# Kernel tuning notes

Measured on AMD Instinct MI355X. Metric: run time of the kernel, lower is better.

The kernel has to match this reference:

```python
import jax, jax.numpy as jnp
import numpy as np

DIM = 1024
NUM_HEADS = 16
HEAD_DIM = DIM // NUM_HEADS
SCALE = HEAD_DIM ** -0.5


def setup_inputs() -> dict:
    key = jax.random.key(0)
    ks = jax.random.split(key, 7)
    b, n = 2, 2048
    x = jax.random.normal(ks[0], (b, n, DIM), dtype=jnp.float32)
    s = DIM ** -0.5
    Wq = jax.random.normal(ks[1], (DIM, DIM), dtype=jnp.float32) * s
    bq = jax.random.normal(ks[2], (DIM,), dtype=jnp.float32) * 0.01
    Wk = jax.random.normal(ks[3], (DIM, DIM), dtype=jnp.float32) * s
    bk = jax.random.normal(ks[4], (DIM,), dtype=jnp.float32) * 0.01
    Wv = jax.random.normal(ks[5], (DIM, DIM), dtype=jnp.float32) * s
    bv = jax.random.normal(ks[6], (DIM,), dtype=jnp.float32) * 0.01
    return {"x": x, "Wq": Wq, "bq": bq, "Wk": Wk, "bk": bk, "Wv": Wv, "bv": bv}


def reference(x, Wq, bq, Wk, bk, Wv, bv):
    b, n, _ = x.shape
    # Linear projections (torch Linear: x @ W.T + b; here W stored as [in, out])
    q = x @ Wq + bq
    k = x @ Wk + bk
    v = x @ Wv + bv
    # split heads: [b, n, h*d] -> [b, h, n, d]
    split = lambda t: t.reshape(b, n, NUM_HEADS, HEAD_DIM).transpose(0, 2, 1, 3)
    q, k, v = split(q), split(k), split(v)
    sim = jnp.einsum('bhid,bhjd->bhij', q, k) * SCALE
    attn = jax.nn.softmax(sim, axis=-1)
    out = jnp.einsum('bhij,bhjd->bhid', attn, v)
    return out.transpose(0, 2, 1, 3).reshape(b, n, DIM)
```

## Files before the change

### kernel.cpp

```cpp
#include <hip/hip_runtime.h>
#include <cstdint>
#include <cstddef>

#define NB    2
#define SEQ   2048
#define DIMC  1024
#define NH    16
#define HDIM  64
#define MROWS (NB*SEQ)
#define NFEAT (3*DIMC)
#define KVBLK 64

typedef _Float16 half8 __attribute__((ext_vector_type(8)));
typedef _Float16 half4 __attribute__((ext_vector_type(4)));
typedef _Float16 half2v __attribute__((ext_vector_type(2)));
typedef __fp16   fp16x2 __attribute__((ext_vector_type(2)));
typedef float    f32x4 __attribute__((ext_vector_type(4)));

typedef const __attribute__((address_space(1))) void* gas_ptr;
typedef __attribute__((address_space(3))) void*       las_ptr;

__device__ __forceinline__ void gload_lds16(const void* g, void* l) {
    __builtin_amdgcn_global_load_lds((gas_ptr)g, (las_ptr)l, 16, 0, 0);
}

__device__ __forceinline__ int swz4(int r) { return (r ^ (r >> 2)) & 3; }

__device__ __forceinline__ float fast_exp2(float x) {
    float r;
    asm("v_exp_f32 %0, %1" : "=v"(r) : "v"(x));
    return r;
}

__device__ __forceinline__ half2v pk_f16(float a, float b) {
    fp16x2 r = __builtin_amdgcn_cvt_pkrtz(a, b);
    return __builtin_bit_cast(half2v, r);
}

__global__ __launch_bounds__(256) void k_prep(const float* __restrict__ x,
                                              const float* __restrict__ Wq,
                                              const float* __restrict__ Wk,
                                              const float* __restrict__ Wv,
                                              _Float16* __restrict__ x16,
                                              _Float16* __restrict__ wt) {
    __shared__ float tile[64][65];
    const int tid = threadIdx.x;
    if (blockIdx.x < 4096) {
        int i = (blockIdx.x * 256 + tid) * 4;
        float4 v = *reinterpret_cast<const float4*>(x + i);
        half4 h = { (_Float16)v.x, (_Float16)v.y, (_Float16)v.z, (_Float16)v.w };
        *reinterpret_cast<half4*>(x16 + i) = h;
        return;
    }
    const int bid  = blockIdx.x - 4096;
    const int midx = bid >> 8;
    const int t2   = bid & 255;
    const int i0   = (t2 >> 4) * 64;
    const int o0   = (t2 & 15) * 64;
    const float* W = (midx == 0) ? Wq : (midx == 1 ? Wk : Wv);
    #pragma unroll
    for (int p = 0; p < 4; ++p) {
        int id = p * 256 + tid;
        int r = id >> 4, c4 = (id & 15) * 4;
        float4 v = *reinterpret_cast<const float4*>(W + (size_t)(i0 + r) * DIMC + o0 + c4);
        tile[r][c4 + 0] = v.x; tile[r][c4 + 1] = v.y;
        tile[r][c4 + 2] = v.z; tile[r][c4 + 3] = v.w;
    }
    __syncthreads();
    #pragma unroll
    for (int p = 0; p < 4; ++p) {
        int id = p * 256 + tid;
        int oc = id >> 4, i4 = (id & 15) * 4;
        half4 h = { (_Float16)tile[i4 + 0][oc], (_Float16)tile[i4 + 1][oc],
                    (_Float16)tile[i4 + 2][oc], (_Float16)tile[i4 + 3][oc] };
        *reinterpret_cast<half4*>(wt + (size_t)(midx * DIMC + o0 + oc) * DIMC + i0 + i4) = h;
    }
}

__global__ __launch_bounds__(256) void k_qkv_gemm(
    const _Float16* __restrict__ x16, const _Float16* __restrict__ wt,
    const float* __restrict__ bq, const float* __restrict__ bk, const float* __restrict__ bv,
    _Float16* __restrict__ q16, _Float16* __restrict__ k16, _Float16* __restrict__ vt16)
{
    __shared__ __align__(16) char sraw[49152];
    const int tid = threadIdx.x;
    const int lane = tid & 63;
    const int w = tid >> 6, wm = w >> 1, wn = w & 1;
    const int lr = lane & 15, lg = lane >> 4;
    const int swzb = (blockIdx.x & 7) * 96 + (blockIdx.x >> 3);
    const int bn = swzb % (NFEAT / 128);
    const int bm = swzb / (NFEAT / 128);
    const int m0 = bm * 128, n0 = bn * 128;

    const f32x4 zero4 = {0.f, 0.f, 0.f, 0.f};
    f32x4 acc[4][4];
    #pragma unroll
    for (int i = 0; i < 4; ++i)
        #pragma unroll
        for (int j = 0; j < 4; ++j) acc[i][j] = zero4;

    auto stage = [&](int buf, int kt) {
        const int k0 = kt * 32;
        char* Adst = sraw + buf * 8192;
        char* Bdst = sraw + 24576 + buf * 8192;
        #pragma unroll
        for (int t = 0; t < 2; ++t) {
            int slot = t * 256 + tid;
            int row = slot >> 2, ch = slot & 3;
            int chg = ch ^ swz4(row);
            gload_lds16(x16 + (size_t)(m0 + row) * DIMC + k0 + chg * 8, Adst + slot * 16);
            gload_lds16(wt  + (size_t)(n0 + row) * DIMC + k0 + chg * 8, Bdst + slot * 16);
        }
    };

    stage(0, 0);
    stage(1, 1);
    for (int kt = 0; kt < DIMC / 32; ++kt) {
        if (kt < DIMC / 32 - 1) asm volatile("s_waitcnt vmcnt(4)" ::: "memory");
        else                    asm volatile("s_waitcnt vmcnt(0)" ::: "memory");
        __builtin_amdgcn_s_barrier();
        if (kt + 2 < DIMC / 32) stage((kt + 2) % 3, kt + 2);
        const char* Ab = sraw + (kt % 3) * 8192;
        const char* Bb = sraw + 24576 + (kt % 3) * 8192;
        half8 af[4], bf[4];
        #pragma unroll
        for (int mb = 0; mb < 4; ++mb) {
            int row = wm * 64 + mb * 16 + lr;
            af[mb] = *(const half8*)(Ab + row * 64 + ((lg ^ swz4(row)) << 4));
        }
        #pragma unroll
        for (int nb = 0; nb < 4; ++nb) {
            int col = wn * 64 + nb * 16 + lr;
            bf[nb] = *(const half8*)(Bb + col * 64 + ((lg ^ swz4(col)) << 4));
        }
        #pragma unroll
        for (int mb = 0; mb < 4; ++mb)
            #pragma unroll
            for (int nb = 0; nb < 4; ++nb)
                acc[mb][nb] = __builtin_amdgcn_mfma_f32_16x16x32_f16(af[mb], bf[nb], acc[mb][nb], 0, 0, 0);
    }

    const int sec = n0 >> 10;
    const float* bias = (sec == 0) ? bq : (sec == 1 ? bk : bv);
    const float scl = (sec == 0) ? 0.125f * 1.44269504088896f : 1.0f;
    float bfv[4];
    #pragma unroll
    for (int nb = 0; nb < 4; ++nb)
        bfv[nb] = bias[(n0 & 1023) + wn * 64 + nb * 16 + lr];

    if (sec < 2) {
        _Float16* dst = (sec == 0) ? q16 : k16;
        #pragma unroll
        for (int mb = 0; mb < 4; ++mb)
            #pragma unroll
            for (int i2 = 0; i2 < 4; ++i2) {
                int rg = m0 + wm * 64 + mb * 16 + lg * 4 + i2;
                int bb = rg >> 11, nn = rg & (SEQ - 1);
                #pragma unroll
                for (int nb = 0; nb < 4; ++nb) {
                    int f1 = (n0 & 1023) + wn * 64 + nb * 16 + lr;
                    int hh = f1 >> 6, dd = f1 & 63;
                    dst[((size_t)(bb * NH + hh) * SEQ + nn) * HDIM + dd] =
                        (_Float16)((acc[mb][nb][i2] + bfv[nb]) * scl);
                }
            }
    } else {
        __syncthreads();
        char* lt = sraw;
        #pragma unroll
        for (int mb = 0; mb < 4; ++mb)
            #pragma unroll
            for (int nb = 0; nb < 4; ++nb) {
                int c  = wn * 64 + nb * 16 + lr;
                int r0 = wm * 64 + mb * 16 + lg * 4;
                half4 hv = { (_Float16)(acc[mb][nb][0] + bfv[nb]),
                             (_Float16)(acc[mb][nb][1] + bfv[nb]),
                             (_Float16)(acc[mb][nb][2] + bfv[nb]),
                             (_Float16)(acc[mb][nb][3] + bfv[nb]) };
                *(half4*)(lt + c * 272 + r0 * 2) = hv;
            }
        __syncthreads();
        #pragma unroll
        for (int p = 0; p < 8; ++p) {
            int id = p * 256 + tid;
            int c = id >> 4, r8 = (id & 15) * 8;
            half8 hv = *(const half8*)(lt + c * 272 + r8 * 2);
            int f1 = (n0 & 1023) + c;
            int hh = f1 >> 6, dd = f1 & 63;
            int rg = m0 + r8;
            int bb = rg >> 11, nn = rg & (SEQ - 1);
            *(half8*)(vt16 + ((size_t)(bb * NH + hh) * HDIM + dd) * SEQ + nn) = hv;
        }
    }
}

__global__ __launch_bounds__(512, 4) void k_attn(
    const _Float16* __restrict__ q16, const _Float16* __restrict__ k16,
    const _Float16* __restrict__ vt16, float* __restrict__ out)
{
    __shared__ __align__(16) char lds[81920];
    const int tid = threadIdx.x, lane = tid & 63, w = tid >> 6;
    const int lr = lane & 15, lg = lane >> 4;
    const int sub = w >> 2;
    const int qg  = w & 3;
    const int swz = (blockIdx.x & 7) * 64 + (blockIdx.x >> 3);
    const int bh = swz >> 4;
    const int qt = swz & 15;
    const int qrow0 = qt * 128 + qg * 32;
    const _Float16* qh = q16 + (size_t)bh * SEQ * HDIM;
    const _Float16* kh = k16 + (size_t)bh * SEQ * HDIM;
    const _Float16* vh = vt16 + (size_t)bh * HDIM * SEQ;
    char* pl = lds + 65536 + w * 2048;
    const int rb = lr >> 3;

    const int srow = tid >> 3;
    const int scg  = (tid & 7) ^ (srow & 7);

    auto stageKV = [&](int buf, int t) {
        const int jA = t * KVBLK, jB = (16 + t) * KVBLK;
        gload_lds16(kh + (size_t)(jA + srow) * HDIM + scg * 8,
                    lds + buf * 8192 + tid * 16);
        gload_lds16(kh + (size_t)(jB + srow) * HDIM + scg * 8,
                    lds + 16384 + buf * 8192 + tid * 16);
        gload_lds16(vh + (size_t)srow * SEQ + jA + scg * 8,
                    lds + 32768 + buf * 8192 + tid * 16);
        gload_lds16(vh + (size_t)srow * SEQ + jB + scg * 8,
                    lds + 49152 + buf * 8192 + tid * 16);
    };

    half8 aq[2][2];
    #pragma unroll
    for (int g = 0; g < 2; ++g)
        #pragma unroll
        for (int kc = 0; kc < 2; ++kc)
            aq[g][kc] = *(const half8*)(qh + (size_t)(qrow0 + g * 16 + lr) * HDIM + kc * 32 + lg * 8);

    const f32x4 zero4 = {0.f, 0.f, 0.f, 0.f};
    f32x4 l4[2] = { zero4, zero4 };
    f32x4 oacc[2][4];
    #pragma unroll
    for (int g = 0; g < 2; ++g)
        #pragma unroll
        for (int i = 0; i < 4; ++i) oacc[g][i] = zero4;

    stageKV(0, 0);
    for (int t = 0; t < 16; ++t) {
        __syncthreads();
        if (t + 1 < 16) stageKV((t + 1) & 1, t + 1);
        const char* Kb = lds + sub * 16384 + (t & 1) * 8192;
        const char* Vb = lds + 32768 + sub * 16384 + (t & 1) * 8192;

        f32x4 s0[4], s1[4];
        __builtin_amdgcn_s_setprio(1);
        #pragma unroll
        for (int jb = 0; jb < 4; ++jb) {
            int row = jb * 16 + lr;
            half8 k0 = *(const half8*)(Kb + row * 128 + (((0 + lg) ^ (row & 7)) << 4));
            half8 k1 = *(const half8*)(Kb + row * 128 + (((4 + lg) ^ (row & 7)) << 4));
            f32x4 a0 = __builtin_amdgcn_mfma_f32_16x16x32_f16(k0, aq[0][0], zero4, 0, 0, 0);
            f32x4 a1 = __builtin_amdgcn_mfma_f32_16x16x32_f16(k0, aq[1][0], zero4, 0, 0, 0);
            a0 = __builtin_amdgcn_mfma_f32_16x16x32_f16(k1, aq[0][1], a0, 0, 0, 0);
            a1 = __builtin_amdgcn_mfma_f32_16x16x32_f16(k1, aq[1][1], a1, 0, 0, 0);
            s0[jb] = a0; s1[jb] = a1;
        }
        __builtin_amdgcn_s_setprio(0);

        #pragma unroll
        for (int jb = 0; jb < 4; ++jb) {
            #pragma unroll
            for (int i = 0; i < 4; ++i) s0[jb][i] = fast_exp2(s0[jb][i]);
            l4[0] += s0[jb];
            half2v w0 = pk_f16(s0[jb][0], s0[jb][1]);
            half2v w1 = pk_f16(s0[jb][2], s0[jb][3]);
            half4 pk = { w0.x, w0.y, w1.x, w1.y };
            *(half4*)(pl + lr * 128 + (((jb * 2 + (lg >> 1)) ^ (lr & 7)) << 4)
                      + (((lg & 1) ^ rb) << 3)) = pk;
        }
        half4 pk1[4];
        #pragma unroll
        for (int jb = 0; jb < 4; ++jb) {
            #pragma unroll
            for (int i = 0; i < 4; ++i) s1[jb][i] = fast_exp2(s1[jb][i]);
            l4[1] += s1[jb];
            half2v w0 = pk_f16(s1[jb][0], s1[jb][1]);
            half2v w1 = pk_f16(s1[jb][2], s1[jb][3]);
            pk1[jb] = half4{ w0.x, w0.y, w1.x, w1.y };
        }
        asm volatile("s_waitcnt lgkmcnt(0)" ::: "memory");
        const char* prow = pl + lr * 128;
        half8 ap[2][2];
        {
            half4 l0 = *(const half4*)(prow + (((0 + lg) ^ (lr & 7)) << 4) + (rb << 3));
            half4 h0 = *(const half4*)(prow + (((0 + lg) ^ (lr & 7)) << 4) + ((1 ^ rb) << 3));
            half4 l1 = *(const half4*)(prow + (((4 + lg) ^ (lr & 7)) << 4) + (rb << 3));
            half4 h1 = *(const half4*)(prow + (((4 + lg) ^ (lr & 7)) << 4) + ((1 ^ rb) << 3));
            ap[0][0] = half8{ l0.x, l0.y, l0.z, l0.w, h0.x, h0.y, h0.z, h0.w };
            ap[0][1] = half8{ l1.x, l1.y, l1.z, l1.w, h1.x, h1.y, h1.z, h1.w };
        }
        #pragma unroll
        for (int jb = 0; jb < 4; ++jb)
            *(half4*)(pl + lr * 128 + (((jb * 2 + (lg >> 1)) ^ (lr & 7)) << 4)
                      + (((lg & 1) ^ rb) << 3)) = pk1[jb];
        asm volatile("s_waitcnt lgkmcnt(0)" ::: "memory");
        {
            half4 l0 = *(const half4*)(prow + (((0 + lg) ^ (lr & 7)) << 4) + (rb << 3));
            half4 h0 = *(const half4*)(prow + (((0 + lg) ^ (lr & 7)) << 4) + ((1 ^ rb) << 3));
            half4 l1 = *(const half4*)(prow + (((4 + lg) ^ (lr & 7)) << 4) + (rb << 3));
            half4 h1 = *(const half4*)(prow + (((4 + lg) ^ (lr & 7)) << 4) + ((1 ^ rb) << 3));
            ap[1][0] = half8{ l0.x, l0.y, l0.z, l0.w, h0.x, h0.y, h0.z, h0.w };
            ap[1][1] = half8{ l1.x, l1.y, l1.z, l1.w, h1.x, h1.y, h1.z, h1.w };
        }
        __builtin_amdgcn_s_setprio(1);
        #pragma unroll
        for (int db = 0; db < 4; ++db) {
            int row = db * 16 + lr;
            half8 vf0 = *(const half8*)(Vb + row * 128 + (((0 + lg) ^ (row & 7)) << 4));
            half8 vf1 = *(const half8*)(Vb + row * 128 + (((4 + lg) ^ (row & 7)) << 4));
            oacc[0][db] = __builtin_amdgcn_mfma_f32_16x16x32_f16(ap[0][0], vf0, oacc[0][db], 0, 0, 0);
            oacc[1][db] = __builtin_amdgcn_mfma_f32_16x16x32_f16(ap[1][0], vf0, oacc[1][db], 0, 0, 0);
            oacc[0][db] = __builtin_amdgcn_mfma_f32_16x16x32_f16(ap[0][1], vf1, oacc[0][db], 0, 0, 0);
            oacc[1][db] = __builtin_amdgcn_mfma_f32_16x16x32_f16(ap[1][1], vf1, oacc[1][db], 0, 0, 0);
        }
        __builtin_amdgcn_s_setprio(0);
    }

    __syncthreads();
    char* xch = lds;
    if (sub == 1) {
        char* sl = xch + (qg * 2) * 5120;
        #pragma unroll
        for (int g = 0; g < 2; ++g) {
            #pragma unroll
            for (int db = 0; db < 4; ++db)
                *(f32x4*)(sl + g * 5120 + db * 1024 + lane * 16) = oacc[g][db];
            *(f32x4*)(sl + g * 5120 + 4096 + lane * 16) = l4[g];
        }
    }
    __syncthreads();
    if (sub == 0) {
        char* sl = xch + (qg * 2) * 5120;
        #pragma unroll
        for (int g = 0; g < 2; ++g) {
            #pragma unroll
            for (int db = 0; db < 4; ++db)
                oacc[g][db] += *(const f32x4*)(sl + g * 5120 + db * 1024 + lane * 16);
            l4[g] += *(const f32x4*)(sl + g * 5120 + 4096 + lane * 16);
        }
        const int bb = bh >> 4, hh = bh & 15;
        #pragma unroll
        for (int g = 0; g < 2; ++g) {
            float l_i = (l4[g][0] + l4[g][1]) + (l4[g][2] + l4[g][3]);
            l_i += __shfl_xor(l_i, 16);
            l_i += __shfl_xor(l_i, 32);
            float rlq[4];
            #pragma unroll
            for (int i = 0; i < 4; ++i)
                rlq[i] = 1.0f / __shfl(l_i, lg * 4 + i);
            #pragma unroll
            for (int db = 0; db < 4; ++db)
                #pragma unroll
                for (int i = 0; i < 4; ++i) {
                    int nn = qrow0 + g * 16 + lg * 4 + i;
                    out[((size_t)bb * SEQ + nn) * DIMC + hh * HDIM + db * 16 + lr] =
                        oacc[g][db][i] * rlq[i];
                }
        }
    }
}

extern "C" void kernel_launch(void* const* d_in, const int* in_sizes, int n_in,
                              void* d_out, int out_size, void* d_ws, size_t ws_size,
                              hipStream_t stream)
{
    const float* x  = (const float*)d_in[0];
    const float* Wq = (const float*)d_in[1];
    const float* bq = (const float*)d_in[2];
    const float* Wk = (const float*)d_in[3];
    const float* bk = (const float*)d_in[4];
    const float* Wv = (const float*)d_in[5];
    const float* bv = (const float*)d_in[6];
    float* out = (float*)d_out;

    char* ws = (char*)d_ws;
    _Float16* x16  = (_Float16*)ws;
    _Float16* wt   = (_Float16*)(ws + ((size_t)8  << 20));
    _Float16* q16  = (_Float16*)(ws + ((size_t)14 << 20));
    _Float16* k16  = (_Float16*)(ws + ((size_t)22 << 20));
    _Float16* vt16 = (_Float16*)(ws + ((size_t)30 << 20));

    k_prep<<<4096 + 768, 256, 0, stream>>>(x, Wq, Wk, Wv, x16, wt);
    k_qkv_gemm<<<(MROWS / 128) * (NFEAT / 128), 256, 0, stream>>>(x16, wt, bq, bk, bv,
                                                                  q16, k16, vt16);
    k_attn<<<32 * (SEQ / 128), 512, 0, stream>>>(q16, k16, vt16, out);
}
```

Before: 91.26 us.

## Enlarge QKV GEMM tiles to 256x256 with 8 waves and K=64 double buffering

Restructures the QKV projection GEMM so each 512-thread block computes a 256x256 output tile, staging K in chunks of 64 with double-buffered LDS and an 8-way XOR swizzle. Global loads for the next stage are interleaved with the MFMA sub-steps, and s_setprio raises wave priority around the MFMA bursts. The aim is more data reuse per LDS load and fewer blocks and barriers per unit of work. In exchange it uses 128KB of LDS and more accumulator registers, launches only 192 blocks (under one wave across the CUs), and splits the V transpose epilogue into two passes.

```diff
diff --git a/kernel.cpp b/kernel.cpp
--- a/kernel.cpp
+++ b/kernel.cpp
@@ -23,8 +23,6 @@
 __device__ __forceinline__ void gload_lds16(const void* g, void* l) {
     __builtin_amdgcn_global_load_lds((gas_ptr)g, (las_ptr)l, 16, 0, 0);
 }
-
-__device__ __forceinline__ int swz4(int r) { return (r ^ (r >> 2)) & 3; }
 
 __device__ __forceinline__ float fast_exp2(float x) {
     float r;
@@ -77,67 +75,81 @@
     }
 }
 
-__global__ __launch_bounds__(256) void k_qkv_gemm(
+__global__ __launch_bounds__(512, 2) void k_qkv_gemm(
     const _Float16* __restrict__ x16, const _Float16* __restrict__ wt,
     const float* __restrict__ bq, const float* __restrict__ bk, const float* __restrict__ bv,
     _Float16* __restrict__ q16, _Float16* __restrict__ k16, _Float16* __restrict__ vt16)
 {
-    __shared__ __align__(16) char sraw[49152];
-    const int tid = threadIdx.x;
-    const int lane = tid & 63;
-    const int w = tid >> 6, wm = w >> 1, wn = w & 1;
+    __shared__ __align__(16) char lds[131072];
+    const int tid = threadIdx.x, lane = tid & 63, w = tid >> 6;
+    const int wm = w >> 2, wn = w & 3;
     const int lr = lane & 15, lg = lane >> 4;
-    const int swzb = (blockIdx.x & 7) * 96 + (blockIdx.x >> 3);
-    const int bn = swzb % (NFEAT / 128);
-    const int bm = swzb / (NFEAT / 128);
-    const int m0 = bm * 128, n0 = bn * 128;
+    const int swzb = (blockIdx.x & 7) * 24 + (blockIdx.x >> 3);
+    const int bn = swzb % (NFEAT / 256);
+    const int bm = swzb / (NFEAT / 256);
+    const int m0 = bm * 256, n0 = bn * 256;
 
     const f32x4 zero4 = {0.f, 0.f, 0.f, 0.f};
-    f32x4 acc[4][4];
-    #pragma unroll
-    for (int i = 0; i < 4; ++i)
+    f32x4 acc[8][4];
+    #pragma unroll
+    for (int i = 0; i < 8; ++i)
         #pragma unroll
         for (int j = 0; j < 4; ++j) acc[i][j] = zero4;
 
-    auto stage = [&](int buf, int kt) {
-        const int k0 = kt * 32;
-        char* Adst = sraw + buf * 8192;
-        char* Bdst = sraw + 24576 + buf * 8192;
-        #pragma unroll
-        for (int t = 0; t < 2; ++t) {
-            int slot = t * 256 + tid;
-            int row = slot >> 2, ch = slot & 3;
-            int chg = ch ^ swz4(row);
-            gload_lds16(x16 + (size_t)(m0 + row) * DIMC + k0 + chg * 8, Adst + slot * 16);
-            gload_lds16(wt  + (size_t)(n0 + row) * DIMC + k0 + chg * 8, Bdst + slot * 16);
-        }
+    auto stage2 = [&](int buf, int kt, int l) {
+        int slot = l * 512 + tid;
+        int row  = slot >> 3;
+        int cg   = (slot & 7) ^ (row & 7);
+        gload_lds16(x16 + (size_t)(m0 + row) * DIMC + kt * 64 + cg * 8,
+                    lds + buf * 32768 + slot * 16);
+        gload_lds16(wt  + (size_t)(n0 + row) * DIMC + kt * 64 + cg * 8,
+                    lds + 65536 + buf * 32768 + slot * 16);
     };
 
-    stage(0, 0);
-    stage(1, 1);
-    for (int kt = 0; kt < DIMC / 32; ++kt) {
-        if (kt < DIMC / 32 - 1) asm volatile("s_waitcnt vmcnt(4)" ::: "memory");
-        else                    asm volatile("s_waitcnt vmcnt(0)" ::: "memory");
+    #pragma unroll
+    for (int l = 0; l < 4; ++l) stage2(0, 0, l);
+
+    half8 bf[4][2];
+    for (int it = 0; it < 16; ++it) {
+        const char* Ab = lds + (it & 1) * 32768;
+        const char* Bb = lds + 65536 + (it & 1) * 32768;
+        asm volatile("s_waitcnt vmcnt(0)" ::: "memory");
         __builtin_amdgcn_s_barrier();
-        if (kt + 2 < DIMC / 32) stage((kt + 2) % 3, kt + 2);
-        const char* Ab = sraw + (kt % 3) * 8192;
-        const char* Bb = sraw + 24576 + (kt % 3) * 8192;
-        half8 af[4], bf[4];
-        #pragma unroll
-        for (int mb = 0; mb < 4; ++mb) {
-            int row = wm * 64 + mb * 16 + lr;
-            af[mb] = *(const half8*)(Ab + row * 64 + ((lg ^ swz4(row)) << 4));
-        }
-        #pragma unroll
-        for (int nb = 0; nb < 4; ++nb) {
-            int col = wn * 64 + nb * 16 + lr;
-            bf[nb] = *(const half8*)(Bb + col * 64 + ((lg ^ swz4(col)) << 4));
-        }
-        #pragma unroll
-        for (int mb = 0; mb < 4; ++mb)
-            #pragma unroll
-            for (int nb = 0; nb < 4; ++nb)
-                acc[mb][nb] = __builtin_amdgcn_mfma_f32_16x16x32_f16(af[mb], bf[nb], acc[mb][nb], 0, 0, 0);
+        #pragma unroll
+        for (int p = 0; p < 4; ++p) {
+            if (it + 1 < 16) stage2((it + 1) & 1, it + 1, p);
+            if (p == 0) {
+                #pragma unroll
+                for (int nb = 0; nb < 4; ++nb) {
+                    int col = wn * 64 + nb * 16 + lr;
+                    #pragma unroll
+                    for (int kk = 0; kk < 2; ++kk)
+                        bf[nb][kk] = *(const half8*)(Bb + col * 128
+                                        + (((kk * 4 + lg) ^ (col & 7)) << 4));
+                }
+            }
+            half8 af[2][2];
+            #pragma unroll
+            for (int m2 = 0; m2 < 2; ++m2) {
+                int row = wm * 128 + (p * 2 + m2) * 16 + lr;
+                #pragma unroll
+                for (int kk = 0; kk < 2; ++kk)
+                    af[m2][kk] = *(const half8*)(Ab + row * 128
+                                    + (((kk * 4 + lg) ^ (row & 7)) << 4));
+            }
+            __builtin_amdgcn_s_setprio(1);
+            #pragma unroll
+            for (int m2 = 0; m2 < 2; ++m2)
+                #pragma unroll
+                for (int nb = 0; nb < 4; ++nb) {
+                    acc[p * 2 + m2][nb] = __builtin_amdgcn_mfma_f32_16x16x32_f16(
+                        af[m2][0], bf[nb][0], acc[p * 2 + m2][nb], 0, 0, 0);
+                    acc[p * 2 + m2][nb] = __builtin_amdgcn_mfma_f32_16x16x32_f16(
+                        af[m2][1], bf[nb][1], acc[p * 2 + m2][nb], 0, 0, 0);
+                }
+            __builtin_amdgcn_s_setprio(0);
+            if (p < 3) __builtin_amdgcn_s_barrier();
+        }
     }
 
     const int sec = n0 >> 10;
@@ -151,10 +163,10 @@
     if (sec < 2) {
         _Float16* dst = (sec == 0) ? q16 : k16;
         #pragma unroll
-        for (int mb = 0; mb < 4; ++mb)
+        for (int mb = 0; mb < 8; ++mb)
             #pragma unroll
             for (int i2 = 0; i2 < 4; ++i2) {
-                int rg = m0 + wm * 64 + mb * 16 + lg * 4 + i2;
+                int rg = m0 + wm * 128 + mb * 16 + lg * 4 + i2;
                 int bb = rg >> 11, nn = rg & (SEQ - 1);
                 #pragma unroll
                 for (int nb = 0; nb < 4; ++nb) {
@@ -166,30 +178,36 @@
             }
     } else {
         __syncthreads();
-        char* lt = sraw;
-        #pragma unroll
-        for (int mb = 0; mb < 4; ++mb)
-            #pragma unroll
-            for (int nb = 0; nb < 4; ++nb) {
-                int c  = wn * 64 + nb * 16 + lr;
-                int r0 = wm * 64 + mb * 16 + lg * 4;
-                half4 hv = { (_Float16)(acc[mb][nb][0] + bfv[nb]),
-                             (_Float16)(acc[mb][nb][1] + bfv[nb]),
-                             (_Float16)(acc[mb][nb][2] + bfv[nb]),
-                             (_Float16)(acc[mb][nb][3] + bfv[nb]) };
-                *(half4*)(lt + c * 272 + r0 * 2) = hv;
+        char* lt = lds;
+        #pragma unroll
+        for (int pass = 0; pass < 2; ++pass) {
+            if (wm == pass) {
+                #pragma unroll
+                for (int mb = 0; mb < 8; ++mb)
+                    #pragma unroll
+                    for (int nb = 0; nb < 4; ++nb) {
+                        int c  = wn * 64 + nb * 16 + lr;
+                        int r0 = mb * 16 + lg * 4;
+                        half4 hv = { (_Float16)(acc[mb][nb][0] + bfv[nb]),
+                                     (_Float16)(acc[mb][nb][1] + bfv[nb]),
+                                     (_Float16)(acc[mb][nb][2] + bfv[nb]),
+                                     (_Float16)(acc[mb][nb][3] + bfv[nb]) };
+                        *(half4*)(lt + c * 272 + r0 * 2) = hv;
+                    }
             }
-        __syncthreads();
-        #pragma unroll
-        for (int p = 0; p < 8; ++p) {
-            int id = p * 256 + tid;
-            int c = id >> 4, r8 = (id & 15) * 8;
-            half8 hv = *(const half8*)(lt + c * 272 + r8 * 2);
-            int f1 = (n0 & 1023) + c;
-            int hh = f1 >> 6, dd = f1 & 63;
-            int rg = m0 + r8;
-            int bb = rg >> 11, nn = rg & (SEQ - 1);
-            *(half8*)(vt16 + ((size_t)(bb * NH + hh) * HDIM + dd) * SEQ + nn) = hv;
+            __syncthreads();
+            #pragma unroll
+            for (int u = 0; u < 8; ++u) {
+                int id = u * 512 + tid;
+                int c = id >> 4, r8 = (id & 15) * 8;
+                half8 hv = *(const half8*)(lt + c * 272 + r8 * 2);
+                int f1 = (n0 & 1023) + c;
+                int hh = f1 >> 6, dd = f1 & 63;
+                int rg = m0 + pass * 128 + r8;
+                int bb = rg >> 11, nn = rg & (SEQ - 1);
+                *(half8*)(vt16 + ((size_t)(bb * NH + hh) * HDIM + dd) * SEQ + nn) = hv;
+            }
+            __syncthreads();
         }
     }
 }
@@ -389,7 +407,7 @@
     _Float16* vt16 = (_Float16*)(ws + ((size_t)30 << 20));
 
     k_prep<<<4096 + 768, 256, 0, stream>>>(x, Wq, Wk, Wv, x16, wt);
-    k_qkv_gemm<<<(MROWS / 128) * (NFEAT / 128), 256, 0, stream>>>(x16, wt, bq, bk, bv,
+    k_qkv_gemm<<<(MROWS / 256) * (NFEAT / 256), 512, 0, stream>>>(x16, wt, bq, bk, bv,
                                                                   q16, k16, vt16);
     k_attn<<<32 * (SEQ / 128), 512, 0, stream>>>(q16, k16, vt16, out);
 }
```

After: 84.38 us, median of 2. 7.5% less time.
